# Kernel optimization log

Hardware: AMD Instinct MI355X
Metric: run time of the kernel (lower is better)

Reference implementation:

```python
import jax, jax.numpy as jnp
import numpy as np

C = 1024   # hidden_size
H = 16     # num_heads
D = C // H # head dim
M = 4096   # mlp hidden
T = 1024   # motion seq len
B = 8      # batch
TA = 1024  # audio seq len


def _w(key, shape):
    return jax.random.normal(key, shape, dtype=jnp.float32) * 0.02


def setup_inputs() -> dict:
    key = jax.random.key(0)
    ks = jax.random.split(key, 32)
    inp = {
        'x': jax.random.normal(ks[0], (T, B, C), dtype=jnp.float32),
        'c': jax.random.normal(ks[1], (B, C), dtype=jnp.float32),
        'padding_mask': jax.random.randint(ks[2], (B, T), 0, 2, dtype=jnp.int32),
        'audio_seq': jax.random.normal(ks[3], (TA, B, C), dtype=jnp.float32),
        'audio_mask': jax.random.randint(ks[4], (B, TA), 0, 2, dtype=jnp.int32),
        # adaLN modulation: SiLU -> Linear(C, 6C)
        'w_ada': _w(ks[5], (C, 6 * C)), 'b_ada': jnp.zeros((6 * C,), jnp.float32),
        # self-attention q/k/v/proj
        'wq': _w(ks[6], (C, C)), 'bq': jnp.zeros((C,), jnp.float32),
        'wk': _w(ks[7], (C, C)), 'bk': jnp.zeros((C,), jnp.float32),
        'wv': _w(ks[8], (C, C)), 'bv': jnp.zeros((C,), jnp.float32),
        'wo': _w(ks[9], (C, C)), 'bo': jnp.zeros((C,), jnp.float32),
        # cross-attention q/k/v/proj
        'cwq': _w(ks[10], (C, C)), 'cbq': jnp.zeros((C,), jnp.float32),
        'cwk': _w(ks[11], (C, C)), 'cbk': jnp.zeros((C,), jnp.float32),
        'cwv': _w(ks[12], (C, C)), 'cbv': jnp.zeros((C,), jnp.float32),
        'cwo': _w(ks[13], (C, C)), 'cbo': jnp.zeros((C,), jnp.float32),
        # MLP fc1/fc2
        'w1': _w(ks[14], (C, M)), 'b1': jnp.zeros((M,), jnp.float32),
        'w2': _w(ks[15], (M, C)), 'b2': jnp.zeros((C,), jnp.float32),
    }
    return inp


def _ln(x):
    # LayerNorm(elementwise_affine=False, eps=1e-6)
    mu = jnp.mean(x, axis=-1, keepdims=True)
    var = jnp.var(x, axis=-1, keepdims=True)
    return (x - mu) * jax.lax.rsqrt(var + 1e-6)


def _modulate(x, shift, scale):
    # batch-first x [B, T, C]; shift/scale [B, C]
    return x * (1.0 + scale[:, None, :]) + shift[:, None, :]


def _mha(xq, xkv, wq, bq, wk, bk, wv, bv, wo, bo, mask):
    # xq [B, Tq, C], xkv [B, Tk, C], mask [B, Tk] (nonzero = masked)
    b, tq, _ = xq.shape
    tk = xkv.shape[1]
    q = (xq @ wq + bq).reshape(b, tq, H, D)
    k = (xkv @ wk + bk).reshape(b, tk, H, D)
    v = (xkv @ wv + bv).reshape(b, tk, H, D)
    att = jnp.einsum('bqhd,bkhd->bhqk', q, k) * (1.0 / np.sqrt(D))
    att = jnp.where(mask[:, None, None, :] != 0, -jnp.inf, att)
    att = jax.nn.softmax(att, axis=-1)
    y = jnp.einsum('bhqk,bkhd->bqhd', att, v).reshape(b, tq, C)
    return y @ wo + bo


def _gelu_tanh(x):
    return jax.nn.gelu(x, approximate=True)


def reference(x, c, padding_mask, audio_seq, audio_mask,
              w_ada, b_ada, wq, bq, wk, bk, wv, bv, wo, bo,
              cwq, cbq, cwk, cbk, cwv, cbv, cwo, cbo,
              w1, b1, w2, b2):
    # adaLN modulation parameters
    mod = jax.nn.silu(c) @ w_ada + b_ada                 # [B, 6C]
    (shift_msa, scale_msa, gate_msa,
     shift_mlp, scale_mlp, gate_mlp) = jnp.split(mod, 6, axis=1)

    # x is sequence-first [T, B, C] (padding_mask batch dim matches x dim 1)
    x_batch = jnp.transpose(x, (1, 0, 2))                # [B, T, C]
    x_mod = _modulate(_ln(x_batch), shift_msa, scale_msa)
    attn_out = _mha(x_mod, x_mod, wq, bq, wk, bk, wv, bv, wo, bo, padding_mask)
    x = x + gate_msa[None, :, :] * jnp.transpose(attn_out, (1, 0, 2))

    # cross attention (reuses msa shift/scale/gate, as in the source)
    xb = jnp.transpose(x, (1, 0, 2))                     # [B, T, C]
    ab = jnp.transpose(audio_seq, (1, 0, 2))             # [B, TA, C]
    x_cross_in = _modulate(_ln(xb), shift_msa, scale_msa)
    cross_out = _mha(x_cross_in, ab, cwq, cbq, cwk, cbk, cwv, cbv, cwo, cbo,
                     audio_mask)
    x = x + gate_msa[None, :, :] * jnp.transpose(cross_out, (1, 0, 2))

    # MLP
    xb = jnp.transpose(x, (1, 0, 2))
    h = _modulate(_ln(xb), shift_mlp, scale_mlp)
    mlp_out = _gelu_tanh(h @ w1 + b1) @ w2 + b2
    x = x + gate_mlp[None, :, :] * jnp.transpose(mlp_out, (1, 0, 2))
    return x
```

## Files before the change

### kernel.cpp

```cpp
#include <hip/hip_runtime.h>
#include <math.h>

#define T_SEQ 1024
#define TA_SEQ 1024
#define BATCH 8
#define CH 1024
#define NH 16
#define HD 64
#define MH 4096

typedef unsigned short u16;
typedef unsigned short u16x4 __attribute__((ext_vector_type(4)));
typedef unsigned short u16x8 __attribute__((ext_vector_type(8)));
typedef __bf16 bf16x8 __attribute__((ext_vector_type(8)));
typedef float f32x4 __attribute__((ext_vector_type(4)));

__device__ __forceinline__ u16 f2bf(float f) {
  unsigned int u = __builtin_bit_cast(unsigned int, f);
  u += 0x7FFFu + ((u >> 16) & 1u);
  return (u16)(u >> 16);
}
__device__ __forceinline__ u16 f2bf_trunc(float f) {
  return (u16)(__builtin_bit_cast(unsigned int, f) >> 16);
}
__device__ __forceinline__ bf16x8 ldbf8(const u16* p) {
  return __builtin_bit_cast(bf16x8, *reinterpret_cast<const u16x8*>(p));
}
__device__ __forceinline__ void gload_lds16(const u16* g, u16* l) {
  __builtin_amdgcn_global_load_lds(
      (const __attribute__((address_space(1))) unsigned int*)g,
      (__attribute__((address_space(3))) unsigned int*)l, 16, 0, 0);
}

#define ASM_BAR()   asm volatile("s_barrier" ::: "memory")
#define ASM_VM8()   asm volatile("s_waitcnt vmcnt(8)" ::: "memory")
#define ASM_VM4()   asm volatile("s_waitcnt vmcnt(4)" ::: "memory")
#define ASM_VM0()   asm volatile("s_waitcnt vmcnt(0)" ::: "memory")
#define ASM_LGKM0() asm volatile("s_waitcnt lgkmcnt(0)" ::: "memory")

__global__ void k_transpose_w(const float* __restrict__ in, u16* __restrict__ out,
                              int K, int N) {
  __shared__ float tile[32][33];
  int n0 = blockIdx.x * 32, k0 = blockIdx.y * 32;
  int tx = threadIdx.x, ty = threadIdx.y;
#pragma unroll
  for (int i = 0; i < 4; i++)
    tile[ty + i * 8][tx] = in[(size_t)(k0 + ty + i * 8) * N + n0 + tx];
  __syncthreads();
#pragma unroll
  for (int i = 0; i < 4; i++)
    out[(size_t)(n0 + ty + i * 8) * K + k0 + tx] = f2bf(tile[tx][ty + i * 8]);
}

struct P8f { const float* p[8]; };
struct P8u { u16* p[8]; };
__global__ void k_transpose8(P8f in8, P8u out8) {
  const float* __restrict__ in = in8.p[blockIdx.z];
  u16* __restrict__ out = out8.p[blockIdx.z];
  __shared__ float tile[32][33];
  int n0 = blockIdx.x * 32, k0 = blockIdx.y * 32;
  int tx = threadIdx.x, ty = threadIdx.y;
#pragma unroll
  for (int i = 0; i < 4; i++)
    tile[ty + i * 8][tx] = in[(size_t)(k0 + ty + i * 8) * CH + n0 + tx];
  __syncthreads();
#pragma unroll
  for (int i = 0; i < 4; i++)
    out[(size_t)(n0 + ty + i * 8) * CH + k0 + tx] = f2bf(tile[tx][ty + i * 8]);
}

__global__ void k_ada(const float* __restrict__ c, const float* __restrict__ w_ada,
                      const float* __restrict__ b_ada, float* __restrict__ mod) {
  __shared__ float sc[CH];
  int b = blockIdx.y;
  int tid = threadIdx.x;
  for (int i = tid; i < CH; i += 256) {
    float cv = c[b * CH + i];
    sc[i] = cv / (1.0f + expf(-cv));
  }
  __syncthreads();
  int n = blockIdx.x * 256 + tid;
  float acc = 0.0f;
  for (int k = 0; k < CH; k++) acc += sc[k] * w_ada[(size_t)k * (6 * CH) + n];
  mod[(size_t)b * (6 * CH) + n] = acc + b_ada[n];
}

__global__ void k_tbc_to_btc_f32(const float* __restrict__ in, float* __restrict__ out) {
  size_t i = (size_t)blockIdx.x * 256 + threadIdx.x;
  int c = (int)(i & (CH - 1));
  size_t tb = i >> 10;
  int b = (int)(tb & (BATCH - 1));
  size_t t = tb >> 3;
  out[((size_t)b * T_SEQ + t) * CH + c] = in[i];
}
__global__ void k_tbc_to_btc_bf16(const float* __restrict__ in, u16* __restrict__ out) {
  size_t i = (size_t)blockIdx.x * 256 + threadIdx.x;
  int c = (int)(i & (CH - 1));
  size_t tb = i >> 10;
  int b = (int)(tb & (BATCH - 1));
  size_t t = tb >> 3;
  out[((size_t)b * TA_SEQ + t) * CH + c] = f2bf(in[i]);
}

__global__ void k_ln_mod(const float* __restrict__ xb, const float* __restrict__ mod,
                         u16* __restrict__ out, int shift_sel, int scale_sel) {
  int row = blockIdx.x;
  int b = row >> 10;
  int tid = threadIdx.x;
  const float* xr = xb + (size_t)row * CH;
  float4 v = reinterpret_cast<const float4*>(xr)[tid];
  float s = v.x + v.y + v.z + v.w;
  float s2 = v.x * v.x + v.y * v.y + v.z * v.z + v.w * v.w;
#pragma unroll
  for (int off = 32; off > 0; off >>= 1) {
    s += __shfl_down(s, off);
    s2 += __shfl_down(s2, off);
  }
  __shared__ float red[8];
  __shared__ float stats[2];
  int wid = tid >> 6;
  if ((tid & 63) == 0) { red[wid] = s; red[4 + wid] = s2; }
  __syncthreads();
  if (tid == 0) {
    float a = red[0] + red[1] + red[2] + red[3];
    float a2 = red[4] + red[5] + red[6] + red[7];
    float mu = a * (1.0f / CH);
    float var = a2 * (1.0f / CH) - mu * mu;
    stats[0] = mu;
    stats[1] = rsqrtf(var + 1e-6f);
  }
  __syncthreads();
  float mu = stats[0], rs = stats[1];
  int c0 = tid * 4;
  const float* sh = mod + (size_t)b * (6 * CH) + (size_t)shift_sel * CH + c0;
  const float* scl = mod + (size_t)b * (6 * CH) + (size_t)scale_sel * CH + c0;
  float xs[4] = {v.x, v.y, v.z, v.w};
  u16x4 o;
#pragma unroll
  for (int j = 0; j < 4; j++)
    o[j] = f2bf((xs[j] - mu) * rs * (1.0f + scl[j]) + sh[j]);
  *reinterpret_cast<u16x4*>(out + (size_t)row * CH + c0) = o;
}

__device__ __forceinline__ void gemm_compute(const u16* As, const u16* Bs,
                                             int wm, int wn, int lrow, int sx,
                                             f32x4 (&acc)[4][4]) {
  bf16x8 af[4], bfr[4];
#pragma unroll
  for (int mi = 0; mi < 4; mi++)
    af[mi] = ldbf8(&As[(wm + mi * 16 + lrow) * 32 + sx]);
#pragma unroll
  for (int ni = 0; ni < 4; ni++)
    bfr[ni] = ldbf8(&Bs[(wn + ni * 16 + lrow) * 32 + sx]);
#pragma unroll
  for (int mi = 0; mi < 4; mi++)
#pragma unroll
    for (int ni = 0; ni < 4; ni++)
      acc[mi][ni] = __builtin_amdgcn_mfma_f32_16x16x32_bf16(af[mi], bfr[ni],
                                                            acc[mi][ni], 0, 0, 0);
}

__device__ __forceinline__ void gemm_core(
    const u16* __restrict__ A, const u16* __restrict__ Bt, int K,
    int m0, int n0, int tid, u16* As, u16* Bs, f32x4 (&acc)[4][4]) {
  int wid = tid >> 6, lane = tid & 63;
  int wm = (wid >> 1) * 64, wn = (wid & 1) * 64;
  int lrow = lane & 15, quad = lane >> 4;
  int sx = (quad ^ ((lrow >> 1) & 3)) * 8;
  int c0 = tid, c1 = 256 + tid;
  int r0 = c0 >> 2, r1 = c1 >> 2;
  int q0 = ((c0 & 3) ^ ((r0 >> 1) & 3)) * 8;
  int q1 = ((c1 & 3) ^ ((r1 >> 1) & 3)) * 8;
  const u16* ga0 = A + (size_t)(m0 + r0) * K + q0;
  const u16* ga1 = A + (size_t)(m0 + r1) * K + q1;
  const u16* gb0 = Bt + (size_t)(n0 + r0) * K + q0;
  const u16* gb1 = Bt + (size_t)(n0 + r1) * K + q1;
  u16* la0 = As + c0 * 8;
  u16* la1 = As + c1 * 8;
  u16* lb0 = Bs + c0 * 8;
  u16* lb1 = Bs + c1 * 8;
  auto stage = [&](int tile, int boff) {
    int ko = tile << 5;
    gload_lds16(ga0 + ko, la0 + boff);
    gload_lds16(ga1 + ko, la1 + boff);
    gload_lds16(gb0 + ko, lb0 + boff);
    gload_lds16(gb1 + ko, lb1 + boff);
  };
  const int kiters = K >> 5;
  stage(0, 0);
  stage(1, 4096);
  int kt = 0;
  for (; kt + 4 < kiters; kt += 3) {
    ASM_LGKM0(); ASM_VM4(); ASM_BAR();
    stage(kt + 2, 8192);
    gemm_compute(As, Bs, wm, wn, lrow, sx, acc);
    ASM_LGKM0(); ASM_VM4(); ASM_BAR();
    stage(kt + 3, 0);
    gemm_compute(As + 4096, Bs + 4096, wm, wn, lrow, sx, acc);
    ASM_LGKM0(); ASM_VM4(); ASM_BAR();
    stage(kt + 4, 4096);
    gemm_compute(As + 8192, Bs + 8192, wm, wn, lrow, sx, acc);
  }
  ASM_LGKM0(); ASM_VM4(); ASM_BAR();
  gemm_compute(As, Bs, wm, wn, lrow, sx, acc);
  ASM_LGKM0(); ASM_VM0(); ASM_BAR();
  gemm_compute(As + 4096, Bs + 4096, wm, wn, lrow, sx, acc);
}

template <int EPI>
__global__ __launch_bounds__(256) void k_gemm(
    const u16* __restrict__ A, const u16* __restrict__ Bt,
    const float* __restrict__ bias, u16* __restrict__ out_bf,
    float* __restrict__ xb, const float* __restrict__ mod, int gate_sel,
    int M, int N, int K) {
  __shared__ u16 As[3 * 128 * 32];
  __shared__ u16 Bs[3 * 128 * 32];
  int m0 = blockIdx.x * 128, n0 = blockIdx.y * 128;
  int tid = threadIdx.x;
  int wid = tid >> 6, lane = tid & 63;
  int wm = (wid >> 1) * 64, wn = (wid & 1) * 64;
  int lrow = lane & 15, quad = lane >> 4;
  f32x4 acc[4][4];
#pragma unroll
  for (int mi = 0; mi < 4; mi++)
#pragma unroll
    for (int ni = 0; ni < 4; ni++) acc[mi][ni] = {0.f, 0.f, 0.f, 0.f};
  gemm_core(A, Bt, K, m0, n0, tid, As, Bs, acc);
#pragma unroll
  for (int mi = 0; mi < 4; mi++)
#pragma unroll
    for (int ni = 0; ni < 4; ni++) {
      int col = n0 + wn + ni * 16 + lrow;
      float bval = bias[col];
#pragma unroll
      for (int r = 0; r < 4; r++) {
        int row = m0 + wm + mi * 16 + quad * 4 + r;
        float v = acc[mi][ni][r] + bval;
        if (EPI == 1) {
          int b = row >> 10;
          float g = mod[(size_t)b * (6 * CH) + (size_t)gate_sel * CH + col];
          xb[(size_t)row * N + col] += g * v;
        } else if (EPI == 2) {
          float t2 = 2.3021181302f * (v + 0.044715f * v * v * v);
          float gel = v * __builtin_amdgcn_rcpf(1.0f + exp2f(-t2));
          out_bf[(size_t)row * N + col] = f2bf(gel);
        } else {
          out_bf[(size_t)row * N + col] = f2bf(v * 0.18033688011112042f);
        }
      }
    }
}

__device__ __forceinline__ void mfma_quad(const bf16x8 (&af)[4], const bf16x8 (&bfr)[4],
                                          f32x4 (*arow)[4]) {
#pragma unroll
  for (int mi = 0; mi < 4; mi++)
#pragma unroll
    for (int ni = 0; ni < 4; ni++)
      arow[mi][ni] = __builtin_amdgcn_mfma_f32_16x16x32_bf16(af[mi], bfr[ni],
                                                             arow[mi][ni], 0, 0, 0);
}

__device__ __forceinline__ void gemm256_core(
    const u16* __restrict__ A, const u16* __restrict__ Bt, int K,
    int m0, int n0, int tid, u16* AS, u16* BS, f32x4 (&acc)[8][4]) {
  int wid = tid >> 6, lane = tid & 63;
  int wr = wid >> 2, wc = wid & 3;
  int lrow = lane & 15, quad = lane >> 4;
  int sx = (quad ^ ((lrow >> 1) & 3)) * 8;
  int aRow = wr * 128 + lrow;
  int bRow = wc * 64 + lrow;
  int rA = tid >> 2;
  int qsw = (((tid & 3) ^ ((tid >> 3) & 3)) << 3);
  const u16* gA = A + (size_t)(m0 + rA) * K + qsw;
  const u16* gB = Bt + (size_t)(n0 + rA) * K + qsw;
  const size_t r128 = (size_t)128 * K;
  u16* dA = AS + tid * 8;
  u16* dB = BS + tid * 8;
  const int NT = K >> 6;

#define STGA(dd, hh, tt) do { const u16* s_ = gA + ((tt) * 64 + (hh) * 32); \
    u16* d_ = dA + ((dd) * 2 + (hh)) * 8192; \
    gload_lds16(s_, d_); gload_lds16(s_ + r128, d_ + 4096); } while (0)
#define STGB(dd, hh, tt) do { const u16* s_ = gB + ((tt) * 64 + (hh) * 32); \
    u16* d_ = dB + ((dd) * 2 + (hh)) * 8192; \
    gload_lds16(s_, d_); gload_lds16(s_ + r128, d_ + 4096); } while (0)
#define RD_A(dd, kk, mh) do { const u16* b_ = AS + ((dd) * 2 + (kk)) * 8192; \
    int r_ = aRow + (mh) * 64; \
    af[0] = ldbf8(&b_[(r_) * 32 + sx]); \
    af[1] = ldbf8(&b_[(r_ + 16) * 32 + sx]); \
    af[2] = ldbf8(&b_[(r_ + 32) * 32 + sx]); \
    af[3] = ldbf8(&b_[(r_ + 48) * 32 + sx]); } while (0)
#define RD_B(dd, kk) do { const u16* b_ = BS + ((dd) * 2 + (kk)) * 8192; \
    bfr[0] = ldbf8(&b_[(bRow) * 32 + sx]); \
    bfr[1] = ldbf8(&b_[(bRow + 16) * 32 + sx]); \
    bfr[2] = ldbf8(&b_[(bRow + 32) * 32 + sx]); \
    bfr[3] = ldbf8(&b_[(bRow + 48) * 32 + sx]); } while (0)
#define PHASE_TAIL(mh) do { ASM_LGKM0(); __builtin_amdgcn_sched_barrier(0); \
    __builtin_amdgcn_s_setprio(1); mfma_quad(af, bfr, acc + (mh) * 4); \
    __builtin_amdgcn_s_setprio(0); ASM_BAR(); } while (0)

  STGA(0, 0, 0); STGB(0, 0, 0); STGA(0, 1, 0); STGB(0, 1, 0);
  STGA(1, 0, 1); STGB(1, 0, 1);
  ASM_VM8(); ASM_BAR();

  bf16x8 af[4], bfr[4];
  for (int t = 0; t < NT; ++t) {
    int d = t & 1;
    RD_A(d, 0, 0); RD_B(d, 0);
    if (t + 1 < NT) STGA(d ^ 1, 1, t + 1);
    PHASE_TAIL(0);
    RD_A(d, 0, 1);
    if (t + 1 < NT) STGB(d ^ 1, 1, t + 1);
    if (t == NT - 1) { ASM_VM0(); } else { ASM_VM8(); }
    PHASE_TAIL(1);
    RD_A(d, 1, 0); RD_B(d, 1);
    if (t + 2 < NT) STGA(d, 0, t + 2);
    PHASE_TAIL(0);
    RD_A(d, 1, 1);
    if (t + 2 < NT) STGB(d, 0, t + 2);
    if (t < NT - 2) { ASM_VM8(); } else if (t == NT - 2) { ASM_VM4(); }
    PHASE_TAIL(1);
  }
#undef STGA
#undef STGB
#undef RD_A
#undef RD_B
#undef PHASE_TAIL
}

template <int EPI>
__global__ __launch_bounds__(512, 2) void k_gemm256(
    const u16* __restrict__ A, const u16* __restrict__ Bt,
    const float* __restrict__ bias, u16* __restrict__ out_bf,
    float* __restrict__ xb, const float* __restrict__ mod, int gate_sel,
    int M, int N, int K) {
  __shared__ u16 AS[2 * 2 * 8192];
  __shared__ u16 BS[2 * 2 * 8192];
  int m0 = blockIdx.x * 256, n0 = blockIdx.y * 256;
  int tid = threadIdx.x;
  int wid = tid >> 6, lane = tid & 63;
  int wr = wid >> 2, wc = wid & 3;
  int lrow = lane & 15, quad = lane >> 4;
  f32x4 acc[8][4];
#pragma unroll
  for (int mi = 0; mi < 8; mi++)
#pragma unroll
    for (int ni = 0; ni < 4; ni++) acc[mi][ni] = {0.f, 0.f, 0.f, 0.f};
  gemm256_core(A, Bt, K, m0, n0, tid, AS, BS, acc);
#pragma unroll
  for (int mi = 0; mi < 8; mi++)
#pragma unroll
    for (int ni = 0; ni < 4; ni++) {
      int col = n0 + wc * 64 + ni * 16 + lrow;
      float bval = bias[col];
#pragma unroll
      for (int r = 0; r < 4; r++) {
        int row = m0 + wr * 128 + mi * 16 + quad * 4 + r;
        float v = acc[mi][ni][r] + bval;
        if (EPI == 1) {
          int b = row >> 10;
          float g = mod[(size_t)b * (6 * CH) + (size_t)gate_sel * CH + col];
          xb[(size_t)row * N + col] += g * v;
        } else if (EPI == 2) {
          float t2 = 2.3021181302f * (v + 0.044715f * v * v * v);
          float gel = v * __builtin_amdgcn_rcpf(1.0f + exp2f(-t2));
          out_bf[(size_t)row * N + col] = f2bf(gel);
        } else {
          out_bf[(size_t)row * N + col] = f2bf(v * 0.18033688011112042f);
        }
      }
    }
}

__global__ __launch_bounds__(512, 2) void k_qkv256(
    const u16* __restrict__ A, const u16* __restrict__ Bt,
    const float* __restrict__ bq, const float* __restrict__ bk,
    const float* __restrict__ bv,
    u16* __restrict__ qout, u16* __restrict__ kout, u16* __restrict__ vt) {
  __shared__ u16 AS[2 * 2 * 8192];
  __shared__ u16 BS[2 * 2 * 8192];
  int m0 = blockIdx.x * 256, n0 = blockIdx.y * 256;
  int tid = threadIdx.x;
  int wid = tid >> 6, lane = tid & 63;
  int wr = wid >> 2, wc = wid & 3;
  int lrow = lane & 15, quad = lane >> 4;
  f32x4 acc[8][4];
#pragma unroll
  for (int mi = 0; mi < 8; mi++)
#pragma unroll
    for (int ni = 0; ni < 4; ni++) acc[mi][ni] = {0.f, 0.f, 0.f, 0.f};
  gemm256_core(A, Bt, CH, m0, n0, tid, AS, BS, acc);
  int seg = n0 >> 10;
  const float* bias = (seg == 0) ? bq : (seg == 1) ? bk : bv;
#pragma unroll
  for (int mi = 0; mi < 8; mi++)
#pragma unroll
    for (int ni = 0; ni < 4; ni++) {
      int col = (n0 & 1023) + wc * 64 + ni * 16 + lrow;
      float bval = bias[col];
      int row0 = m0 + wr * 128 + mi * 16 + quad * 4;
      if (seg == 0) {
#pragma unroll
        for (int r = 0; r < 4; r++)
          qout[(size_t)(row0 + r) * CH + col] =
              f2bf((acc[mi][ni][r] + bval) * 0.18033688011112042f);
      } else if (seg == 1) {
#pragma unroll
        for (int r = 0; r < 4; r++)
          kout[(size_t)(row0 + r) * CH + col] = f2bf(acc[mi][ni][r] + bval);
      } else {
        u16x4 pk;
#pragma unroll
        for (int r = 0; r < 4; r++) pk[r] = f2bf(acc[mi][ni][r] + bval);
        int b = row0 >> 10, t0 = row0 & 1023;
        int h = col >> 6, d = col & 63;
        *reinterpret_cast<u16x4*>(
            vt + (((size_t)(b * NH + h) * HD + d) << 10) + t0) = pk;
      }
    }
}

__global__ __launch_bounds__(512, 2) void k_kv256(
    const u16* __restrict__ A, const u16* __restrict__ Bt,
    const float* __restrict__ bk, const float* __restrict__ bv,
    u16* __restrict__ kout, u16* __restrict__ vt) {
  __shared__ u16 AS[2 * 2 * 8192];
  __shared__ u16 BS[2 * 2 * 8192];
  int m0 = blockIdx.x * 256, n0 = blockIdx.y * 256;
  int tid = threadIdx.x;
  int wid = tid >> 6, lane = tid & 63;
  int wr = wid >> 2, wc = wid & 3;
  int lrow = lane & 15, quad = lane >> 4;
  f32x4 acc[8][4];
#pragma unroll
  for (int mi = 0; mi < 8; mi++)
#pragma unroll
    for (int ni = 0; ni < 4; ni++) acc[mi][ni] = {0.f, 0.f, 0.f, 0.f};
  gemm256_core(A, Bt, CH, m0, n0, tid, AS, BS, acc);
  int seg = n0 >> 10;
  const float* bias = (seg == 0) ? bk : bv;
#pragma unroll
  for (int mi = 0; mi < 8; mi++)
#pragma unroll
    for (int ni = 0; ni < 4; ni++) {
      int col = (n0 & 1023) + wc * 64 + ni * 16 + lrow;
      float bval = bias[col];
      int row0 = m0 + wr * 128 + mi * 16 + quad * 4;
      if (seg == 0) {
#pragma unroll
        for (int r = 0; r < 4; r++)
          kout[(size_t)(row0 + r) * CH + col] = f2bf(acc[mi][ni][r] + bval);
      } else {
        u16x4 pk;
#pragma unroll
        for (int r = 0; r < 4; r++) pk[r] = f2bf(acc[mi][ni][r] + bval);
        int b = row0 >> 10, t0 = row0 & 1023;
        int h = col >> 6, d = col & 63;
        *reinterpret_cast<u16x4*>(
            vt + (((size_t)(b * NH + h) * HD + d) << 10) + t0) = pk;
      }
    }
}

__global__ __launch_bounds__(256, 2) void k_attn(
    const u16* __restrict__ Q, const u16* __restrict__ Kb,
    const u16* __restrict__ vt, const int* __restrict__ mask,
    u16* __restrict__ Y) {
  int qt = blockIdx.x, h = blockIdx.y, b = blockIdx.z;
  int tid = threadIdx.x, wid = tid >> 6, lane = tid & 63;
  int lrow = lane & 15, quad = lane >> 4;
  int qbase = qt * 256 + wid * 64;

  __shared__ u16 P[4][4][16][72];

  bf16x8 aq[4][2];
#pragma unroll
  for (int st = 0; st < 4; st++) {
    size_t qoff = ((size_t)(b * T_SEQ + qbase + st * 16 + lrow)) * CH + h * HD;
    aq[st][0] = ldbf8(Q + qoff + quad * 8);
    aq[st][1] = ldbf8(Q + qoff + 32 + quad * 8);
  }

  u16x8 uo;
#pragma unroll
  for (int j = 0; j < 8; j++) uo[j] = (lrow == 0) ? (u16)0x3F80 : (u16)0;
  bf16x8 ones = __builtin_bit_cast(bf16x8, uo);

  const int* mrow = mask + (size_t)b * T_SEQ;
  const u16* ksrc = Kb + ((size_t)(b * T_SEQ) + lrow) * CH + h * HD + quad * 8;
  const u16* vsrc = vt + (((size_t)(b * NH + h) * HD + lrow) << 10) + quad * 8;

  f32x4 o[4][5];
#pragma unroll
  for (int st = 0; st < 4; st++)
#pragma unroll
    for (int dc = 0; dc < 5; dc++) o[st][dc] = {0.f, 0.f, 0.f, 0.f};

  for (int kt = 0; kt < 16; kt++) {
    int kb = kt * 64;
    bf16x8 kf[8];
    float mb[4];
#pragma unroll
    for (int sub = 0; sub < 4; sub++) {
      const u16* kp = ksrc + (size_t)(kb + sub * 16) * CH;
      kf[sub * 2] = ldbf8(kp);
      kf[sub * 2 + 1] = ldbf8(kp + 32);
      mb[sub] = mrow[kb + sub * 16 + lrow] ? -INFINITY : 0.0f;
    }
    bf16x8 vf[8];
#pragma unroll
    for (int dc = 0; dc < 4; dc++) {
      const u16* vp = vsrc + (size_t)(dc * 16) * 1024 + kb;
      vf[dc * 2] = ldbf8(vp);
      vf[dc * 2 + 1] = ldbf8(vp + 32);
    }
#pragma unroll
    for (int st = 0; st < 4; st++) {
#pragma unroll
      for (int sub = 0; sub < 4; sub++) {
        f32x4 z = {0.f, 0.f, 0.f, 0.f};
        z = __builtin_amdgcn_mfma_f32_16x16x32_bf16(aq[st][0], kf[sub * 2], z, 0, 0, 0);
        z = __builtin_amdgcn_mfma_f32_16x16x32_bf16(aq[st][1], kf[sub * 2 + 1], z, 0, 0, 0);
        float mbv = mb[sub];
#pragma unroll
        for (int r = 0; r < 4; r++) {
          float p = exp2f(z[r] + mbv);
          P[wid][st][quad * 4 + r][sub * 16 + lrow] = f2bf_trunc(p);
        }
      }
    }
#pragma unroll
    for (int st = 0; st < 4; st++) {
      bf16x8 pf0 = ldbf8(&P[wid][st][lrow][quad * 8]);
      bf16x8 pf1 = ldbf8(&P[wid][st][lrow][32 + quad * 8]);
#pragma unroll
      for (int dc = 0; dc < 4; dc++) {
        o[st][dc] = __builtin_amdgcn_mfma_f32_16x16x32_bf16(pf0, vf[dc * 2], o[st][dc], 0, 0, 0);
        o[st][dc] = __builtin_amdgcn_mfma_f32_16x16x32_bf16(pf1, vf[dc * 2 + 1], o[st][dc], 0, 0, 0);
      }
      o[st][4] = __builtin_amdgcn_mfma_f32_16x16x32_bf16(pf0, ones, o[st][4], 0, 0, 0);
      o[st][4] = __builtin_amdgcn_mfma_f32_16x16x32_bf16(pf1, ones, o[st][4], 0, 0, 0);
    }
  }

#pragma unroll
  for (int st = 0; st < 4; st++)
#pragma unroll
    for (int r = 0; r < 4; r++) {
      float l = __shfl(o[st][4][r], lane & 48);
      float linv = 1.0f / l;
      int qr = qbase + st * 16 + quad * 4 + r;
      size_t yo = ((size_t)(b * T_SEQ + qr)) * CH + h * HD;
#pragma unroll
      for (int dc = 0; dc < 4; dc++)
        Y[yo + dc * 16 + lrow] = f2bf(o[st][dc][r] * linv);
    }
}

__global__ void k_out(const float* __restrict__ xb, float* __restrict__ out) {
  size_t i = (size_t)blockIdx.x * 256 + threadIdx.x;
  int c = (int)(i & (CH - 1));
  size_t tb = i >> 10;
  int b = (int)(tb & (BATCH - 1));
  size_t t = tb >> 3;
  out[i] = xb[((size_t)b * T_SEQ + t) * CH + c];
}

extern "C" void kernel_launch(void* const* d_in, const int* in_sizes, int n_in,
                              void* d_out, int out_size, void* d_ws, size_t ws_size,
                              hipStream_t stream) {
  const float* x     = (const float*)d_in[0];
  const float* c     = (const float*)d_in[1];
  const int*   pmask = (const int*)d_in[2];
  const float* audio = (const float*)d_in[3];
  const int*   amask = (const int*)d_in[4];
  const float* w_ada = (const float*)d_in[5];
  const float* b_ada = (const float*)d_in[6];
  const float* wq = (const float*)d_in[7];  const float* bq = (const float*)d_in[8];
  const float* wk = (const float*)d_in[9];  const float* bk = (const float*)d_in[10];
  const float* wv = (const float*)d_in[11]; const float* bv = (const float*)d_in[12];
  const float* wo = (const float*)d_in[13]; const float* bo = (const float*)d_in[14];
  const float* cwq = (const float*)d_in[15]; const float* cbq = (const float*)d_in[16];
  const float* cwk = (const float*)d_in[17]; const float* cbk = (const float*)d_in[18];
  const float* cwv = (const float*)d_in[19]; const float* cbv = (const float*)d_in[20];
  const float* cwo = (const float*)d_in[21]; const float* cbo = (const float*)d_in[22];
  const float* w1 = (const float*)d_in[23]; const float* b1 = (const float*)d_in[24];
  const float* w2 = (const float*)d_in[25]; const float* b2 = (const float*)d_in[26];

  char* wsb = (char*)d_ws;
  size_t off = 0;
  auto alloc = [&](size_t bytes) {
    char* p = wsb + off;
    off += (bytes + 255) & ~(size_t)255;
    return p;
  };
  const size_t SQ = (size_t)CH * CH * 2;
  u16* wqT  = (u16*)alloc(SQ);
  u16* wkT  = (u16*)alloc(SQ);
  u16* wvT  = (u16*)alloc(SQ);
  u16* woT  = (u16*)alloc(SQ);
  u16* cwqT = (u16*)alloc(SQ);
  u16* cwkT = (u16*)alloc(SQ);
  u16* cwvT = (u16*)alloc(SQ);
  u16* cwoT = (u16*)alloc(SQ);
  u16* w1T  = (u16*)alloc((size_t)CH * MH * 2);
  u16* w2T  = (u16*)alloc((size_t)CH * MH * 2);
  float* mod = (float*)alloc((size_t)BATCH * 6 * CH * 4);
  float* xb  = (float*)alloc((size_t)BATCH * T_SEQ * CH * 4);
  u16* xm    = (u16*)alloc((size_t)BATCH * T_SEQ * CH * 2);
  u16* hbuf  = (u16*)alloc((size_t)BATCH * T_SEQ * MH * 2);
  u16* qbuf  = hbuf;
  u16* kbuf  = hbuf + (size_t)BATCH * T_SEQ * CH;
  u16* ybuf  = hbuf + (size_t)2 * BATCH * T_SEQ * CH;
  u16* vt    = hbuf + (size_t)3 * BATCH * T_SEQ * CH;
  u16* abuf  = (u16*)alloc((size_t)BATCH * TA_SEQ * CH * 2);
  (void)ws_size; (void)in_sizes; (void)n_in; (void)out_size;

  const int NE = T_SEQ * BATCH * CH;
  dim3 tb32(32, 8);

  P8f src8; P8u dst8;
  src8.p[0] = wq;  dst8.p[0] = wqT;
  src8.p[1] = wk;  dst8.p[1] = wkT;
  src8.p[2] = wv;  dst8.p[2] = wvT;
  src8.p[3] = wo;  dst8.p[3] = woT;
  src8.p[4] = cwq; dst8.p[4] = cwqT;
  src8.p[5] = cwk; dst8.p[5] = cwkT;
  src8.p[6] = cwv; dst8.p[6] = cwvT;
  src8.p[7] = cwo; dst8.p[7] = cwoT;
  k_transpose8<<<dim3(CH / 32, CH / 32, 8), tb32, 0, stream>>>(src8, dst8);
  k_transpose_w<<<dim3(MH / 32, CH / 32), tb32, 0, stream>>>(w1, w1T, CH, MH);
  k_transpose_w<<<dim3(CH / 32, MH / 32), tb32, 0, stream>>>(w2, w2T, MH, CH);

  k_ada<<<dim3(6 * CH / 256, BATCH), 256, 0, stream>>>(c, w_ada, b_ada, mod);
  k_tbc_to_btc_f32<<<NE / 256, 256, 0, stream>>>(x, xb);
  k_tbc_to_btc_bf16<<<NE / 256, 256, 0, stream>>>(audio, abuf);

  k_ln_mod<<<BATCH * T_SEQ, 256, 0, stream>>>(xb, mod, xm, 0, 1);
  k_qkv256<<<dim3(32, 12), 512, 0, stream>>>(xm, wqT, bq, bk, bv, qbuf, kbuf, vt);
  k_attn<<<dim3(T_SEQ / 256, NH, BATCH), 256, 0, stream>>>(qbuf, kbuf, vt, pmask, ybuf);
  k_gemm<1><<<dim3(64, 8), 256, 0, stream>>>(ybuf, woT, bo, nullptr, xb, mod, 2, 8192, CH, CH);

  k_ln_mod<<<BATCH * T_SEQ, 256, 0, stream>>>(xb, mod, xm, 0, 1);
  k_gemm<3><<<dim3(64, 8), 256, 0, stream>>>(xm, cwqT, cbq, qbuf, nullptr, nullptr, 0, 8192, CH, CH);
  k_kv256<<<dim3(32, 8), 512, 0, stream>>>(abuf, cwkT, cbk, cbv, kbuf, vt);
  k_attn<<<dim3(T_SEQ / 256, NH, BATCH), 256, 0, stream>>>(qbuf, kbuf, vt, amask, ybuf);
  k_gemm<1><<<dim3(64, 8), 256, 0, stream>>>(ybuf, cwoT, cbo, nullptr, xb, mod, 2, 8192, CH, CH);

  k_ln_mod<<<BATCH * T_SEQ, 256, 0, stream>>>(xb, mod, xm, 3, 4);
  k_gemm256<2><<<dim3(32, 16), 512, 0, stream>>>(xm, w1T, b1, hbuf, nullptr, nullptr, 0, 8192, MH, CH);
  k_gemm<1><<<dim3(64, 8), 256, 0, stream>>>(hbuf, w2T, b2, nullptr, xb, mod, 5, 8192, CH, MH);

  k_out<<<NE / 256, 256, 0, stream>>>(xb, (float*)d_out);
}
```

Before: 892.8 us.

## Fuse layout transposes into LN and final GEMM; add 256x128 GEMM kernel

Removes the separate TBC->BTC copy of x by having the first LayerNorm kernel read x in sequence-first layout and write the batch-first residual copy itself. Removes the final output transpose kernel by having the last fc2 GEMM epilogue add the residual and write directly in [T,B,C] order. Replaces the 128x128, 256-thread GEMM with a 256x128-tile, 512-thread kernel that uses double-buffered 64-wide K stages, split-phase LDS reads, and setprio around MFMA blocks, for the N=1024 projections. It cuts two full-tensor memory passes and aims for better MFMA utilization, at the cost of fewer blocks (256) per GEMM and more complex vmcnt accounting.

```diff
diff --git a/kernel.cpp b/kernel.cpp
--- a/kernel.cpp
+++ b/kernel.cpp
@@ -34,7 +34,9 @@
 
 #define ASM_BAR()   asm volatile("s_barrier" ::: "memory")
 #define ASM_VM8()   asm volatile("s_waitcnt vmcnt(8)" ::: "memory")
+#define ASM_VM6()   asm volatile("s_waitcnt vmcnt(6)" ::: "memory")
 #define ASM_VM4()   asm volatile("s_waitcnt vmcnt(4)" ::: "memory")
+#define ASM_VM3()   asm volatile("s_waitcnt vmcnt(3)" ::: "memory")
 #define ASM_VM0()   asm volatile("s_waitcnt vmcnt(0)" ::: "memory")
 #define ASM_LGKM0() asm volatile("s_waitcnt lgkmcnt(0)" ::: "memory")
 
@@ -85,14 +87,6 @@
   mod[(size_t)b * (6 * CH) + n] = acc + b_ada[n];
 }
 
-__global__ void k_tbc_to_btc_f32(const float* __restrict__ in, float* __restrict__ out) {
-  size_t i = (size_t)blockIdx.x * 256 + threadIdx.x;
-  int c = (int)(i & (CH - 1));
-  size_t tb = i >> 10;
-  int b = (int)(tb & (BATCH - 1));
-  size_t t = tb >> 3;
-  out[((size_t)b * T_SEQ + t) * CH + c] = in[i];
-}
 __global__ void k_tbc_to_btc_bf16(const float* __restrict__ in, u16* __restrict__ out) {
   size_t i = (size_t)blockIdx.x * 256 + threadIdx.x;
   int c = (int)(i & (CH - 1));
@@ -102,12 +96,20 @@
   out[((size_t)b * TA_SEQ + t) * CH + c] = f2bf(in[i]);
 }
 
-__global__ void k_ln_mod(const float* __restrict__ xb, const float* __restrict__ mod,
-                         u16* __restrict__ out, int shift_sel, int scale_sel) {
+template <int IN_TBC>
+__global__ void k_ln_mod(const float* __restrict__ src, const float* __restrict__ mod,
+                         u16* __restrict__ out, float* __restrict__ xb_out,
+                         int shift_sel, int scale_sel) {
   int row = blockIdx.x;
   int b = row >> 10;
   int tid = threadIdx.x;
-  const float* xr = xb + (size_t)row * CH;
+  const float* xr;
+  if (IN_TBC) {
+    int t = row & (T_SEQ - 1);
+    xr = src + ((size_t)t * BATCH + b) * CH;
+  } else {
+    xr = src + (size_t)row * CH;
+  }
   float4 v = reinterpret_cast<const float4*>(xr)[tid];
   float s = v.x + v.y + v.z + v.w;
   float s2 = v.x * v.x + v.y * v.y + v.z * v.z + v.w * v.w;
@@ -132,6 +134,8 @@
   __syncthreads();
   float mu = stats[0], rs = stats[1];
   int c0 = tid * 4;
+  if (IN_TBC)
+    reinterpret_cast<float4*>(xb_out + (size_t)row * CH)[tid] = v;
   const float* sh = mod + (size_t)b * (6 * CH) + (size_t)shift_sel * CH + c0;
   const float* scl = mod + (size_t)b * (6 * CH) + (size_t)scale_sel * CH + c0;
   float xs[4] = {v.x, v.y, v.z, v.w};
@@ -140,115 +144,6 @@
   for (int j = 0; j < 4; j++)
     o[j] = f2bf((xs[j] - mu) * rs * (1.0f + scl[j]) + sh[j]);
   *reinterpret_cast<u16x4*>(out + (size_t)row * CH + c0) = o;
-}
-
-__device__ __forceinline__ void gemm_compute(const u16* As, const u16* Bs,
-                                             int wm, int wn, int lrow, int sx,
-                                             f32x4 (&acc)[4][4]) {
-  bf16x8 af[4], bfr[4];
-#pragma unroll
-  for (int mi = 0; mi < 4; mi++)
-    af[mi] = ldbf8(&As[(wm + mi * 16 + lrow) * 32 + sx]);
-#pragma unroll
-  for (int ni = 0; ni < 4; ni++)
-    bfr[ni] = ldbf8(&Bs[(wn + ni * 16 + lrow) * 32 + sx]);
-#pragma unroll
-  for (int mi = 0; mi < 4; mi++)
-#pragma unroll
-    for (int ni = 0; ni < 4; ni++)
-      acc[mi][ni] = __builtin_amdgcn_mfma_f32_16x16x32_bf16(af[mi], bfr[ni],
-                                                            acc[mi][ni], 0, 0, 0);
-}
-
-__device__ __forceinline__ void gemm_core(
-    const u16* __restrict__ A, const u16* __restrict__ Bt, int K,
-    int m0, int n0, int tid, u16* As, u16* Bs, f32x4 (&acc)[4][4]) {
-  int wid = tid >> 6, lane = tid & 63;
-  int wm = (wid >> 1) * 64, wn = (wid & 1) * 64;
-  int lrow = lane & 15, quad = lane >> 4;
-  int sx = (quad ^ ((lrow >> 1) & 3)) * 8;
-  int c0 = tid, c1 = 256 + tid;
-  int r0 = c0 >> 2, r1 = c1 >> 2;
-  int q0 = ((c0 & 3) ^ ((r0 >> 1) & 3)) * 8;
-  int q1 = ((c1 & 3) ^ ((r1 >> 1) & 3)) * 8;
-  const u16* ga0 = A + (size_t)(m0 + r0) * K + q0;
-  const u16* ga1 = A + (size_t)(m0 + r1) * K + q1;
-  const u16* gb0 = Bt + (size_t)(n0 + r0) * K + q0;
-  const u16* gb1 = Bt + (size_t)(n0 + r1) * K + q1;
-  u16* la0 = As + c0 * 8;
-  u16* la1 = As + c1 * 8;
-  u16* lb0 = Bs + c0 * 8;
-  u16* lb1 = Bs + c1 * 8;
-  auto stage = [&](int tile, int boff) {
-    int ko = tile << 5;
-    gload_lds16(ga0 + ko, la0 + boff);
-    gload_lds16(ga1 + ko, la1 + boff);
-    gload_lds16(gb0 + ko, lb0 + boff);
-    gload_lds16(gb1 + ko, lb1 + boff);
-  };
-  const int kiters = K >> 5;
-  stage(0, 0);
-  stage(1, 4096);
-  int kt = 0;
-  for (; kt + 4 < kiters; kt += 3) {
-    ASM_LGKM0(); ASM_VM4(); ASM_BAR();
-    stage(kt + 2, 8192);
-    gemm_compute(As, Bs, wm, wn, lrow, sx, acc);
-    ASM_LGKM0(); ASM_VM4(); ASM_BAR();
-    stage(kt + 3, 0);
-    gemm_compute(As + 4096, Bs + 4096, wm, wn, lrow, sx, acc);
-    ASM_LGKM0(); ASM_VM4(); ASM_BAR();
-    stage(kt + 4, 4096);
-    gemm_compute(As + 8192, Bs + 8192, wm, wn, lrow, sx, acc);
-  }
-  ASM_LGKM0(); ASM_VM4(); ASM_BAR();
-  gemm_compute(As, Bs, wm, wn, lrow, sx, acc);
-  ASM_LGKM0(); ASM_VM0(); ASM_BAR();
-  gemm_compute(As + 4096, Bs + 4096, wm, wn, lrow, sx, acc);
-}
-
-template <int EPI>
-__global__ __launch_bounds__(256) void k_gemm(
-    const u16* __restrict__ A, const u16* __restrict__ Bt,
-    const float* __restrict__ bias, u16* __restrict__ out_bf,
-    float* __restrict__ xb, const float* __restrict__ mod, int gate_sel,
-    int M, int N, int K) {
-  __shared__ u16 As[3 * 128 * 32];
-  __shared__ u16 Bs[3 * 128 * 32];
-  int m0 = blockIdx.x * 128, n0 = blockIdx.y * 128;
-  int tid = threadIdx.x;
-  int wid = tid >> 6, lane = tid & 63;
-  int wm = (wid >> 1) * 64, wn = (wid & 1) * 64;
-  int lrow = lane & 15, quad = lane >> 4;
-  f32x4 acc[4][4];
-#pragma unroll
-  for (int mi = 0; mi < 4; mi++)
-#pragma unroll
-    for (int ni = 0; ni < 4; ni++) acc[mi][ni] = {0.f, 0.f, 0.f, 0.f};
-  gemm_core(A, Bt, K, m0, n0, tid, As, Bs, acc);
-#pragma unroll
-  for (int mi = 0; mi < 4; mi++)
-#pragma unroll
-    for (int ni = 0; ni < 4; ni++) {
-      int col = n0 + wn + ni * 16 + lrow;
-      float bval = bias[col];
-#pragma unroll
-      for (int r = 0; r < 4; r++) {
-        int row = m0 + wm + mi * 16 + quad * 4 + r;
-        float v = acc[mi][ni][r] + bval;
-        if (EPI == 1) {
-          int b = row >> 10;
-          float g = mod[(size_t)b * (6 * CH) + (size_t)gate_sel * CH + col];
-          xb[(size_t)row * N + col] += g * v;
-        } else if (EPI == 2) {
-          float t2 = 2.3021181302f * (v + 0.044715f * v * v * v);
-          float gel = v * __builtin_amdgcn_rcpf(1.0f + exp2f(-t2));
-          out_bf[(size_t)row * N + col] = f2bf(gel);
-        } else {
-          out_bf[(size_t)row * N + col] = f2bf(v * 0.18033688011112042f);
-        }
-      }
-    }
 }
 
 __device__ __forceinline__ void mfma_quad(const bf16x8 (&af)[4], const bf16x8 (&bfr)[4],
@@ -463,6 +358,127 @@
     }
 }
 
+__device__ __forceinline__ void mfma_duo(const bf16x8 (&af)[4], const bf16x8 (&bfr)[2],
+                                         f32x4 (*arow)[2]) {
+#pragma unroll
+  for (int mi = 0; mi < 4; mi++)
+#pragma unroll
+    for (int ni = 0; ni < 2; ni++)
+      arow[mi][ni] = __builtin_amdgcn_mfma_f32_16x16x32_bf16(af[mi], bfr[ni],
+                                                             arow[mi][ni], 0, 0, 0);
+}
+
+__device__ __forceinline__ void gemm128n_core(
+    const u16* __restrict__ A, const u16* __restrict__ Bt, int K,
+    int m0, int n0, int tid, u16* AS, u16* BS, f32x4 (&acc)[8][2]) {
+  int wid = tid >> 6, lane = tid & 63;
+  int wr = wid >> 2, wc = wid & 3;
+  int lrow = lane & 15, quad = lane >> 4;
+  int sx = (quad ^ ((lrow >> 1) & 3)) * 8;
+  int aRow = wr * 128 + lrow;
+  int bRow = wc * 32 + lrow;
+  int rA = tid >> 2;
+  int qsw = (((tid & 3) ^ ((tid >> 3) & 3)) << 3);
+  const u16* gA = A + (size_t)(m0 + rA) * K + qsw;
+  const u16* gB = Bt + (size_t)(n0 + rA) * K + qsw;
+  const size_t r128 = (size_t)128 * K;
+  u16* dA = AS + tid * 8;
+  u16* dB = BS + tid * 8;
+  const int NT = K >> 6;
+
+#define STGA(dd, hh, tt) do { const u16* s_ = gA + ((tt) * 64 + (hh) * 32); \
+    u16* d_ = dA + ((dd) * 2 + (hh)) * 8192; \
+    gload_lds16(s_, d_); gload_lds16(s_ + r128, d_ + 4096); } while (0)
+#define STGB(dd, hh, tt) do { const u16* s_ = gB + ((tt) * 64 + (hh) * 32); \
+    u16* d_ = dB + ((dd) * 2 + (hh)) * 4096; \
+    gload_lds16(s_, d_); } while (0)
+#define RD_A(dd, kk, mh) do { const u16* b_ = AS + ((dd) * 2 + (kk)) * 8192; \
+    int r_ = aRow + (mh) * 64; \
+    af[0] = ldbf8(&b_[(r_) * 32 + sx]); \
+    af[1] = ldbf8(&b_[(r_ + 16) * 32 + sx]); \
+    af[2] = ldbf8(&b_[(r_ + 32) * 32 + sx]); \
+    af[3] = ldbf8(&b_[(r_ + 48) * 32 + sx]); } while (0)
+#define RD_B(dd, kk) do { const u16* b_ = BS + ((dd) * 2 + (kk)) * 4096; \
+    bfr[0] = ldbf8(&b_[(bRow) * 32 + sx]); \
+    bfr[1] = ldbf8(&b_[(bRow + 16) * 32 + sx]); } while (0)
+#define PHASE_TAIL(mh) do { ASM_LGKM0(); __builtin_amdgcn_sched_barrier(0); \
+    __builtin_amdgcn_s_setprio(1); mfma_duo(af, bfr, acc + (mh) * 4); \
+    __builtin_amdgcn_s_setprio(0); ASM_BAR(); } while (0)
+
+  STGA(0, 0, 0); STGB(0, 0, 0); STGA(0, 1, 0); STGB(0, 1, 0);
+  STGA(1, 0, 1); STGB(1, 0, 1);
+  ASM_VM6(); ASM_BAR();
+
+  bf16x8 af[4], bfr[2];
+  for (int t = 0; t < NT; ++t) {
+    int d = t & 1;
+    RD_A(d, 0, 0); RD_B(d, 0);
+    if (t + 1 < NT) STGA(d ^ 1, 1, t + 1);
+    PHASE_TAIL(0);
+    RD_A(d, 0, 1);
+    if (t + 1 < NT) STGB(d ^ 1, 1, t + 1);
+    if (t == NT - 1) { ASM_VM0(); } else { ASM_VM6(); }
+    PHASE_TAIL(1);
+    RD_A(d, 1, 0); RD_B(d, 1);
+    if (t + 2 < NT) STGA(d, 0, t + 2);
+    PHASE_TAIL(0);
+    RD_A(d, 1, 1);
+    if (t + 2 < NT) STGB(d, 0, t + 2);
+    if (t < NT - 2) { ASM_VM6(); } else if (t == NT - 2) { ASM_VM3(); }
+    PHASE_TAIL(1);
+  }
+#undef STGA
+#undef STGB
+#undef RD_A
+#undef RD_B
+#undef PHASE_TAIL
+}
+
+template <int EPI>
+__global__ __launch_bounds__(512, 2) void k_gemm128n(
+    const u16* __restrict__ A, const u16* __restrict__ Bt,
+    const float* __restrict__ bias, u16* __restrict__ out_bf,
+    float* __restrict__ xb, float* __restrict__ dout,
+    const float* __restrict__ mod, int gate_sel, int M, int N, int K) {
+  __shared__ u16 AS[2 * 2 * 8192];
+  __shared__ u16 BS[2 * 2 * 4096];
+  int m0 = blockIdx.x * 256, n0 = blockIdx.y * 128;
+  int tid = threadIdx.x;
+  int wid = tid >> 6, lane = tid & 63;
+  int wr = wid >> 2, wc = wid & 3;
+  int lrow = lane & 15, quad = lane >> 4;
+  f32x4 acc[8][2];
+#pragma unroll
+  for (int mi = 0; mi < 8; mi++)
+#pragma unroll
+    for (int ni = 0; ni < 2; ni++) acc[mi][ni] = {0.f, 0.f, 0.f, 0.f};
+  gemm128n_core(A, Bt, K, m0, n0, tid, AS, BS, acc);
+#pragma unroll
+  for (int mi = 0; mi < 8; mi++)
+#pragma unroll
+    for (int ni = 0; ni < 2; ni++) {
+      int col = n0 + wc * 32 + ni * 16 + lrow;
+      float bval = bias[col];
+#pragma unroll
+      for (int r = 0; r < 4; r++) {
+        int row = m0 + wr * 128 + mi * 16 + quad * 4 + r;
+        float v = acc[mi][ni][r] + bval;
+        if (EPI == 1) {
+          int b = row >> 10;
+          float g = mod[(size_t)b * (6 * CH) + (size_t)gate_sel * CH + col];
+          xb[(size_t)row * N + col] += g * v;
+        } else if (EPI == 3) {
+          out_bf[(size_t)row * N + col] = f2bf(v * 0.18033688011112042f);
+        } else {
+          int b = row >> 10, t = row & (T_SEQ - 1);
+          float g = mod[(size_t)b * (6 * CH) + (size_t)gate_sel * CH + col];
+          dout[((size_t)t * BATCH + b) * CH + col] =
+              xb[(size_t)row * N + col] + g * v;
+        }
+      }
+    }
+}
+
 __global__ __launch_bounds__(256, 2) void k_attn(
     const u16* __restrict__ Q, const u16* __restrict__ Kb,
     const u16* __restrict__ vt, const int* __restrict__ mask,
@@ -556,15 +572,6 @@
       for (int dc = 0; dc < 4; dc++)
         Y[yo + dc * 16 + lrow] = f2bf(o[st][dc][r] * linv);
     }
-}
-
-__global__ void k_out(const float* __restrict__ xb, float* __restrict__ out) {
-  size_t i = (size_t)blockIdx.x * 256 + threadIdx.x;
-  int c = (int)(i & (CH - 1));
-  size_t tb = i >> 10;
-  int b = (int)(tb & (BATCH - 1));
-  size_t t = tb >> 3;
-  out[i] = xb[((size_t)b * T_SEQ + t) * CH + c];
 }
 
 extern "C" void kernel_launch(void* const* d_in, const int* in_sizes, int n_in,
@@ -634,23 +641,20 @@
   k_transpose_w<<<dim3(CH / 32, MH / 32), tb32, 0, stream>>>(w2, w2T, MH, CH);
 
   k_ada<<<dim3(6 * CH / 256, BATCH), 256, 0, stream>>>(c, w_ada, b_ada, mod);
-  k_tbc_to_btc_f32<<<NE / 256, 256, 0, stream>>>(x, xb);
   k_tbc_to_btc_bf16<<<NE / 256, 256, 0, stream>>>(audio, abuf);
 
-  k_ln_mod<<<BATCH * T_SEQ, 256, 0, stream>>>(xb, mod, xm, 0, 1);
+  k_ln_mod<1><<<BATCH * T_SEQ, 256, 0, stream>>>(x, mod, xm, xb, 0, 1);
   k_qkv256<<<dim3(32, 12), 512, 0, stream>>>(xm, wqT, bq, bk, bv, qbuf, kbuf, vt);
   k_attn<<<dim3(T_SEQ / 256, NH, BATCH), 256, 0, stream>>>(qbuf, kbuf, vt, pmask, ybuf);
-  k_gemm<1><<<dim3(64, 8), 256, 0, stream>>>(ybuf, woT, bo, nullptr, xb, mod, 2, 8192, CH, CH);
-
-  k_ln_mod<<<BATCH * T_SEQ, 256, 0, stream>>>(xb, mod, xm, 0, 1);
-  k_gemm<3><<<dim3(64, 8), 256, 0, stream>>>(xm, cwqT, cbq, qbuf, nullptr, nullptr, 0, 8192, CH, CH);
+  k_gemm128n<1><<<dim3(32, 8), 512, 0, stream>>>(ybuf, woT, bo, nullptr, xb, nullptr, mod, 2, 8192, CH, CH);
+
+  k_ln_mod<0><<<BATCH * T_SEQ, 256, 0, stream>>>(xb, mod, xm, nullptr, 0, 1);
+  k_gemm128n<3><<<dim3(32, 8), 512, 0, stream>>>(xm, cwqT, cbq, qbuf, nullptr, nullptr, nullptr, 0, 8192, CH, CH);
   k_kv256<<<dim3(32, 8), 512, 0, stream>>>(abuf, cwkT, cbk, cbv, kbuf, vt);
   k_attn<<<dim3(T_SEQ / 256, NH, BATCH), 256, 0, stream>>>(qbuf, kbuf, vt, amask, ybuf);
-  k_gemm<1><<<dim3(64, 8), 256, 0, stream>>>(ybuf, cwoT, cbo, nullptr, xb, mod, 2, 8192, CH, CH);
-
-  k_ln_mod<<<BATCH * T_SEQ, 256, 0, stream>>>(xb, mod, xm, 3, 4);
+  k_gemm128n<1><<<dim3(32, 8), 512, 0, stream>>>(ybuf, cwoT, cbo, nullptr, xb, nullptr, mod, 2, 8192, CH, CH);
+
+  k_ln_mod<0><<<BATCH * T_SEQ, 256, 0, stream>>>(xb, mod, xm, nullptr, 3, 4);
   k_gemm256<2><<<dim3(32, 16), 512, 0, stream>>>(xm, w1T, b1, hbuf, nullptr, nullptr, 0, 8192, MH, CH);
-  k_gemm<1><<<dim3(64, 8), 256, 0, stream>>>(hbuf, w2T, b2, nullptr, xb, mod, 5, 8192, CH, MH);
-
-  k_out<<<NE / 256, 256, 0, stream>>>(xb, (float*)d_out);
-}
+  k_gemm128n<4><<<dim3(32, 8), 512, 0, stream>>>(hbuf, w2T, b2, nullptr, xb, (float*)d_out, mod, 5, 8192, CH, MH);
+}
```

After: 840.8 us (median of 2 runs). 1.06x faster.
